# Kernel tuning notes

Measured on AMD Instinct MI355X. Metric: run time of the kernel, lower is better.

## Reference

```python
import jax, jax.numpy as jnp
import numpy as np
import math

D_MODEL = 384
D_HEAD = 64
N_HEADS = D_MODEL // D_HEAD  # 6
COND = 768
KSIZE = 7
EPS = 1e-6


def setup_inputs() -> dict:
    key = jax.random.key(0)
    ks = jax.random.split(key, 8)
    n, h, w = 4, 128, 128
    x = jax.random.normal(ks[0], (n, h, w, D_MODEL), jnp.float32)
    pos = jax.random.uniform(ks[1], (n, h, w, 2), jnp.float32)
    cond = jax.random.normal(ks[2], (n, COND), jnp.float32)
    # AdaRMSNorm linear (zero-init in original; small random so it exercises the math)
    w_cond = jax.random.normal(ks[3], (COND, D_MODEL), jnp.float32) * 0.02
    w_qkv = jax.random.normal(ks[4], (D_MODEL, 3 * D_MODEL), jnp.float32) * (D_MODEL ** -0.5)
    scale = jnp.full((N_HEADS,), 10.0, jnp.float32)
    # AxialRoPE freqs: exp(linspace(log(pi), log(10pi), n_heads*dim//4+1)[:-1]).view(dim//4, nh).T
    dim = D_HEAD // 2
    freqs = jnp.exp(jnp.linspace(math.log(math.pi), math.log(10.0 * math.pi),
                                 N_HEADS * (dim // 4) + 1)[:-1])
    freqs = freqs.reshape(dim // 4, N_HEADS).T  # [n_heads, d_head//8]
    w_out = jax.random.normal(ks[5], (D_MODEL, D_MODEL), jnp.float32) * 0.02
    return {"x": x, "pos": pos, "cond": cond, "w_cond": w_cond, "w_qkv": w_qkv,
            "scale": scale, "freqs": freqs, "w_out": w_out}


def rms_norm(x, scale):
    return x * jax.lax.rsqrt(jnp.mean(x * x, axis=-1, keepdims=True) + EPS) * scale


def apply_rotary(x, theta):
    # rotate the first 2*d channels of the head dim, leave the rest untouched
    d = theta.shape[-1]
    x1, x2, x3 = x[..., :d], x[..., d:2 * d], x[..., 2 * d:]
    c, s = jnp.cos(theta), jnp.sin(theta)
    return jnp.concatenate([x1 * c - x2 * s, x2 * c + x1 * s, x3], axis=-1)


def nb_idx(L):
    # NATTEN clamped neighborhood: window start = clip(i - k//2, 0, L-k)
    start = jnp.clip(jnp.arange(L) - KSIZE // 2, 0, L - KSIZE)
    return start[None, :] + jnp.arange(KSIZE)[:, None]  # [KSIZE, L]


def reference(x, pos, cond, w_cond, w_qkv, scale, freqs, w_out):
    n, H, W, _ = x.shape
    skip = x
    # AdaRMSNorm
    x = rms_norm(x, (cond @ w_cond)[:, None, None, :] + 1.0)
    # QKV projection, 'n h w (t nh e) -> t n nh h w e'
    qkv = (x @ w_qkv).reshape(n, H, W, 3, N_HEADS, D_HEAD)
    qkv = jnp.transpose(qkv, (3, 0, 4, 1, 2, 5))
    q, k, v = qkv[0], qkv[1], qkv[2]  # [n, nh, H, W, e]
    # cosine-sim scaling with learned per-head scale
    sq = jnp.sqrt(scale)[:, None, None, None]
    q = q * (sq * jax.lax.rsqrt(jnp.sum(q * q, axis=-1, keepdims=True) + EPS))
    k = k * (sq * jax.lax.rsqrt(jnp.sum(k * k, axis=-1, keepdims=True) + EPS))
    # axial RoPE: theta [n,H,W,nh,d_head//4] per axis -> cat -> movedim(-2,-4)
    th = pos[..., None, 0:1] * freqs
    tw = pos[..., None, 1:2] * freqs
    theta = jnp.moveaxis(jnp.concatenate([th, tw], axis=-1), -2, -4)  # [n,nh,H,W,dd]
    q = apply_rotary(q, theta)
    k = apply_rotary(k, theta)
    # neighborhood attention (na2d_qk / softmax / na2d_av), dilation 1
    ih_all = nb_idx(H)  # [k, H]
    iw_all = nb_idx(W)  # [k, W]
    hh = jnp.repeat(jnp.arange(KSIZE), KSIZE)
    ww = jnp.tile(jnp.arange(KSIZE), KSIZE)
    idx_h = ih_all[hh]  # [k*k, H]
    idx_w = iw_all[ww]  # [k*k, W]

    def qk_step(_, hw):
        ih, iw = hw
        ks_ = k[:, :, ih, :, :][:, :, :, iw, :]  # keys at this window offset
        return None, jnp.einsum('nchwe,nchwe->nchw', q, ks_)

    _, qk = jax.lax.scan(qk_step, None, (idx_h, idx_w))  # [k*k, n, nh, H, W]
    a = jax.nn.softmax(qk, axis=0)  # softmax over the k*k window

    def av_step(acc, inp):
        (ih, iw), at = inp
        vs = v[:, :, ih, :, :][:, :, :, iw, :]
        return acc + at[..., None] * vs, None

    out, _ = jax.lax.scan(av_step, jnp.zeros_like(v), ((idx_h, idx_w), a))
    # 'n nh h w e -> n h w (nh e)'
    out = jnp.transpose(out, (0, 2, 3, 1, 4)).reshape(n, H, W, N_HEADS * D_HEAD)
    return out @ w_out + skip
```

## Files before the change

### kernel.cpp

```cpp
#include <hip/hip_runtime.h>
#include <hip/hip_bf16.h>

#define DM 384
#define NH 6
#define DH 64
#define CD 768
#define NBATCH 4
#define IMH 128
#define IMW 128
#define HEADPIX (IMH*IMW)
#define NPIX (NBATCH*IMH*IMW)
#define PLANE ((size_t)NPIX*DM)
#define KS 7
#define EPSF 1e-6f

typedef __attribute__((ext_vector_type(8))) short bf16x8v;
typedef __attribute__((ext_vector_type(4))) short bf16x4v;
typedef __attribute__((ext_vector_type(4))) float f32x4v;
typedef __attribute__((ext_vector_type(4))) unsigned short u16x4;

#define GLOAD_LDS16(g, l) __builtin_amdgcn_global_load_lds( \
    (const __attribute__((address_space(1))) void*)(g), \
    (__attribute__((address_space(3))) void*)(l), 16, 0, 0)

#define TR64(dst, p, imm) asm volatile("ds_read_b64_tr_b16 %0, %1 offset:" #imm \
    : "=v"(dst) : "v"((const __attribute__((address_space(3))) char*)(p)))

__device__ __forceinline__ unsigned short f2bf(float f){
    __hip_bfloat16 h = __float2bfloat16(f);
    return *reinterpret_cast<unsigned short*>(&h);
}
__device__ __forceinline__ bf16x8v cat8(bf16x4v lo, bf16x4v hi){
    bf16x8v r;
    r[0]=lo[0]; r[1]=lo[1]; r[2]=lo[2]; r[3]=lo[3];
    r[4]=hi[0]; r[5]=hi[1]; r[6]=hi[2]; r[7]=hi[3];
    return r;
}

__device__ __forceinline__ bf16x8v frag8(const __hip_bfloat16* base, int row, int kelem){
    int byteoff = row*128 + ((kelem*2) ^ ((row & 7) << 4));
    return *(const bf16x8v*)((const char*)base + byteoff);
}
__device__ __forceinline__ bf16x8v frag512(const char* base, int row, int kelem){
    int byteoff = row*512 + ((kelem*2) ^ ((row & 7) << 4));
    return *(const bf16x8v*)(base + byteoff);
}

__global__ __launch_bounds__(256) void k_cond(const float* __restrict__ cond,
                                              const float* __restrict__ wc,
                                              float* __restrict__ sc){
    __shared__ float red[4][64];
    const int b = blockIdx.x;
    const int n = b / 6, j0 = (b - n*6) * 64;
    const int lane = threadIdx.x & 63, wave = threadIdx.x >> 6;
    const float* cr = cond + n*CD + wave*192;
    const float* wp = wc + (size_t)(wave*192)*DM + j0 + lane;
    float acc = 0.f;
    #pragma unroll 4
    for (int i = 0; i < 192; ++i) acc += cr[i] * wp[(size_t)i*DM];
    red[wave][lane] = acc;
    __syncthreads();
    if (threadIdx.x < 64) {
        float s = red[0][lane] + red[1][lane] + red[2][lane] + red[3][lane];
        sc[n*DM + j0 + lane] = s + 1.0f;
    }
}

__global__ __launch_bounds__(256) void k_xscale(const float* __restrict__ x,
                                                const float* __restrict__ sc,
                                                __hip_bfloat16* __restrict__ xb){
    int row  = blockIdx.x*4 + (threadIdx.x>>6);
    int lane = threadIdx.x & 63;
    int n    = row >> 14;
    const float* xr  = x + (size_t)row*DM;
    const float* scp = sc + n*DM;
    float v[6];
    float s = 0.f;
    #pragma unroll
    for (int i=0;i<6;++i){ v[i] = xr[i*64+lane]; s += v[i]*v[i]; }
    #pragma unroll
    for (int o=32;o;o>>=1) s += __shfl_xor(s,o);
    float r = rsqrtf(s*(1.0f/DM) + EPSF);
    #pragma unroll
    for (int i=0;i<6;++i)
        xb[(size_t)row*DM + i*64+lane] = __float2bfloat16(v[i]*r*scp[i*64+lane]);
}

__global__ void k_cvtwq(const float* __restrict__ wq, __hip_bfloat16* __restrict__ wqb){
    int id = blockIdx.x*256 + threadIdx.x;
    if (id >= 3*DM*DM) return;
    int nn = id / DM, kk = id - nn*DM;
    wqb[id] = __float2bfloat16(wq[(size_t)kk*(3*DM) + nn]);
}
__global__ void k_cvtwo(const float* __restrict__ wo, __hip_bfloat16* __restrict__ wob){
    int id = blockIdx.x*256 + threadIdx.x;
    if (id >= DM*DM) return;
    int nn = id / DM, kk = id - nn*DM;
    wob[id] = __float2bfloat16(wo[(size_t)kk*DM + nn]);
}

__global__ __launch_bounds__(256) void k_qkv_mfma(
    const __hip_bfloat16* __restrict__ xb, const __hip_bfloat16* __restrict__ wqb,
    const float* __restrict__ pos, const float* __restrict__ freqs,
    const float* __restrict__ scale, __hip_bfloat16* __restrict__ qkv)
{
    __shared__ char As[2*16384];
    __shared__ char Bs[2*16384];
    const int t    = threadIdx.x;
    const int lane = t & 63;
    const int wave = t >> 6;
    const int swzb = (blockIdx.x & 7)*576 + (blockIdx.x >> 3);
    const int jb = swzb % 9;
    const int mb = swzb / 9;
    const int j0 = jb*128, m0 = mb*128;
    const int n  = m0 >> 14;
    const int wr = (wave >> 1) * 64;
    const int wc = (wave & 1) * 64;
    const int fr = lane & 15;
    const int fg = lane >> 4;

    f32x4v acc[4][4] = {};

#define STAGE_QKV(buf, k0) \
    { _Pragma("unroll") \
      for (int i = 0; i < 4; ++i) { \
        int off = (i*256 + t) * 8; \
        int row = off >> 6; \
        int col = (off & 63) ^ ((row & 7) << 3); \
        GLOAD_LDS16(xb  + (size_t)(m0 + row)*DM + (k0) + col, \
                    As + (buf)*16384 + (i*256 + (wave<<6))*16); \
        GLOAD_LDS16(wqb + (size_t)(j0 + row)*DM + (k0) + col, \
                    Bs + (buf)*16384 + (i*256 + (wave<<6))*16); \
      } }

    STAGE_QKV(0, 0)
    #pragma unroll
    for (int kt = 0; kt < 6; ++kt) {
        const int cur = kt & 1;
        if (kt < 5) {
            STAGE_QKV(cur ^ 1, (kt+1)*64)
            asm volatile("s_waitcnt vmcnt(8)" ::: "memory");
        } else {
            asm volatile("s_waitcnt vmcnt(0)" ::: "memory");
        }
        asm volatile("s_barrier" ::: "memory");
        const __hip_bfloat16* Ab = (const __hip_bfloat16*)(As + cur*16384);
        const __hip_bfloat16* Bb = (const __hip_bfloat16*)(Bs + cur*16384);
        #pragma unroll
        for (int kk = 0; kk < 64; kk += 32) {
            bf16x8v af[4], bfr[4];
            #pragma unroll
            for (int i = 0; i < 4; ++i) af[i]  = frag8(Ab, wr + i*16 + fr, kk + fg*8);
            #pragma unroll
            for (int i = 0; i < 4; ++i) bfr[i] = frag8(Bb, wc + i*16 + fr, kk + fg*8);
            #pragma unroll
            for (int i = 0; i < 4; ++i)
            #pragma unroll
            for (int j = 0; j < 4; ++j)
                acc[i][j] = __builtin_amdgcn_mfma_f32_16x16x32_bf16(bfr[i], af[j], acc[i][j], 0, 0, 0);
        }
        asm volatile("s_barrier" ::: "memory");
    }
#undef STAGE_QKV

    const int t_ = jb / 3;
    const int pj = jb - t_*3;
    const int c  = pj*2 + (wc >> 6);
    const size_t hbase = (size_t)t_*PLANE + (((size_t)(n*NH + c)*HEADPIX) << 6);

    if (t_ < 2) {
        const float sq = sqrtf(scale[c]);
        const float4 f4 = *(const float4*)(freqs + c*8 + ((fg & 1) << 2));
        float fqv[4] = {f4.x, f4.y, f4.z, f4.w};
        #pragma unroll
        for (int ni = 0; ni < 4; ++ni) {
            int m = m0 + wr + ni*16 + fr;
            float ss = 0.f;
            #pragma unroll
            for (int i = 0; i < 4; ++i)
                #pragma unroll
                for (int r = 0; r < 4; ++r) ss += acc[i][ni][r]*acc[i][ni][r];
            ss += __shfl_xor(ss, 16);
            ss += __shfl_xor(ss, 32);
            float rn = sq * rsqrtf(ss + EPSF);
            float2 pp = *(const float2*)(pos + (size_t)m*2);
            float pc = (fg < 2) ? pp.x : pp.y;
            u16x4 o0, o1, o2, o3;
            #pragma unroll
            for (int r = 0; r < 4; ++r) {
                float th = pc * fqv[r];
                float ct = __cosf(th), st = __sinf(th);
                float a0 = acc[0][ni][r]*rn, a1 = acc[1][ni][r]*rn;
                o0[r] = f2bf(a0*ct - a1*st);
                o1[r] = f2bf(a1*ct + a0*st);
                o2[r] = f2bf(acc[2][ni][r]*rn);
                o3[r] = f2bf(acc[3][ni][r]*rn);
            }
            size_t base = hbase + ((size_t)(m & (HEADPIX-1)) << 6) + (fg << 2);
            *(u16x4*)(qkv + base     ) = o0;
            *(u16x4*)(qkv + base + 16) = o1;
            *(u16x4*)(qkv + base + 32) = o2;
            *(u16x4*)(qkv + base + 48) = o3;
        }
    } else {
        #pragma unroll
        for (int ni = 0; ni < 4; ++ni) {
            int m = m0 + wr + ni*16 + fr;
            size_t base = hbase + ((size_t)(m & (HEADPIX-1)) << 6) + (fg << 2);
            #pragma unroll
            for (int i = 0; i < 4; ++i) {
                u16x4 pk;
                #pragma unroll
                for (int r = 0; r < 4; ++r) pk[r] = f2bf(acc[i][ni][r]);
                *(u16x4*)(qkv + base + i*16) = pk;
            }
        }
    }
}

__global__ __launch_bounds__(256) void k_attn2(
    const __hip_bfloat16* __restrict__ q, const __hip_bfloat16* __restrict__ kbuf,
    const __hip_bfloat16* __restrict__ vbuf, __hip_bfloat16* __restrict__ attn)
{
    __shared__ char smem[61440];
    char* KP = smem;
    char* VT = smem + 32768;

    const int t    = threadIdx.x;
    const int lane = t & 63;
    const int wave = t >> 6;
    const int fr   = lane & 15;
    const int fg   = lane >> 4;

    const int tile = blockIdx.x;
    const int n6c  = blockIdx.y;
    const int h0 = (tile >> 4) << 3;
    const int w0 = (tile & 15) << 3;
    const int nn = n6c / NH;
    const int cc = n6c - nn*NH;

    const size_t pixbase = (size_t)n6c << 14;
    const __hip_bfloat16* qp = q    + (pixbase << 6);
    const __hip_bfloat16* kp = kbuf + (pixbase << 6);
    const __hip_bfloat16* vp = vbuf + (pixbase << 6);

    const int u0h = min(max(h0-3,0), IMH-7);
    const int u0w = min(max(w0-3,0), IMW-7);

    #pragma unroll
    for (int it = 0; it < 7; ++it) {
        int chunk = it*256 + t;
        int key  = chunk >> 3;
        int part = chunk & 7;
        int kh = min(u0h + (key >> 4), IMH-1);
        int kw = min(u0w + (key & 15), IMW-1);
        GLOAD_LDS16(kp + (((size_t)kh*IMW + kw) << 6) + ((part ^ (key & 7)) << 3),
                    KP + (it*256 + (wave<<6))*16);
    }
    #pragma unroll
    for (int it = 0; it < 7; ++it) {
        int chunk = it*256 + t;
        int keyq = chunk >> 5;
        int rem  = chunk & 31;
        int key  = (keyq << 2) + ((rem >> 1) & 3);
        int d0   = ((rem >> 3) << 4) + ((chunk & 1) << 3);
        int kh = min(u0h + (key >> 4), IMH-1);
        int kw = min(u0w + (key & 15), IMW-1);
        GLOAD_LDS16(vp + (((size_t)kh*IMW + kw) << 6) + d0,
                    VT + (it*256 + (wave<<6))*16);
    }
    const int q_l = (wave<<4) + fr;
    const int qh = h0 + (q_l >> 3), qw = w0 + (q_l & 7);
    const __hip_bfloat16* qrow = qp + (((size_t)qh*IMW + qw) << 6);
    bf16x8v aq0 = *(const bf16x8v*)(qrow + fg*8);
    bf16x8v aq1 = *(const bf16x8v*)(qrow + 32 + fg*8);

    int loh[4], low_[4];
    #pragma unroll
    for (int r = 0; r < 4; ++r) {
        int qr  = (wave<<4) + fg*4 + r;
        int qhr = h0 + (qr >> 3), qwr = w0 + (qr & 7);
        loh[r]  = min(max(qhr-3,0), IMH-7) - u0h;
        low_[r] = min(max(qwr-3,0), IMW-7) - u0w;
    }

    __syncthreads();

    f32x4v acc_s[14];
    #pragma unroll
    for (int nf = 0; nf < 14; ++nf) {
        bf16x8v b0 = frag8((const __hip_bfloat16*)KP, nf*16 + fr, fg*8);
        bf16x8v b1 = frag8((const __hip_bfloat16*)KP, nf*16 + fr, 32 + fg*8);
        f32x4v s = {0.f,0.f,0.f,0.f};
        s = __builtin_amdgcn_mfma_f32_16x16x32_bf16(aq0, b0, s, 0, 0, 0);
        s = __builtin_amdgcn_mfma_f32_16x16x32_bf16(aq1, b1, s, 0, 0, 0);
        acc_s[nf] = s;
    }

    float rs[4] = {0.f,0.f,0.f,0.f};
    #pragma unroll
    for (int nf = 0; nf < 14; ++nf) {
        int key = nf*16 + fr;
        int uh = key >> 4;
        int uw = key & 15;
        #pragma unroll
        for (int r = 0; r < 4; ++r) {
            bool ok = ((unsigned)(uh - loh[r]) <= 6u) && ((unsigned)(uw - low_[r]) <= 6u);
            float pv = ok ? __expf(acc_s[nf][r]) : 0.f;
            acc_s[nf][r] = pv;
            rs[r] += pv;
        }
    }
    #pragma unroll
    for (int o = 1; o < 16; o <<= 1) {
        #pragma unroll
        for (int r = 0; r < 4; ++r) rs[r] += __shfl_xor(rs[r], o);
    }
    float rinv[4];
    #pragma unroll
    for (int r = 0; r < 4; ++r) rinv[r] = 1.0f / rs[r];

    __syncthreads();

    #pragma unroll
    for (int nf = 0; nf < 14; ++nf) {
        int key = nf*16 + fr;
        #pragma unroll
        for (int r = 0; r < 4; ++r) {
            int qr = (wave<<4) + fg*4 + r;
            *(__hip_bfloat16*)(KP + qr*512 + ((key*2) ^ ((qr & 7) << 4))) = __float2bfloat16(acc_s[nf][r]);
        }
    }
    __syncthreads();

    f32x4v acc_o[4] = {};
    const char* vlane = VT + ((lane >> 4) << 10) + ((lane & 15) << 3);
    #pragma unroll
    for (int kst = 0; kst < 7; ++kst) {
        bf16x8v a = frag512(KP, (wave<<4) + fr, kst*32 + fg*8);
        const char* vk = vlane + kst*4096;
        bf16x4v t0a, t0b, t1a, t1b, t2a, t2b, t3a, t3b;
        TR64(t0a, vk,   0); TR64(t0b, vk, 512);
        TR64(t1a, vk, 128); TR64(t1b, vk, 640);
        TR64(t2a, vk, 256); TR64(t2b, vk, 768);
        TR64(t3a, vk, 384); TR64(t3b, vk, 896);
        asm volatile("s_waitcnt lgkmcnt(0)" ::: "memory");
        __builtin_amdgcn_sched_barrier(0);
        acc_o[0] = __builtin_amdgcn_mfma_f32_16x16x32_bf16(a, cat8(t0a,t0b), acc_o[0], 0, 0, 0);
        acc_o[1] = __builtin_amdgcn_mfma_f32_16x16x32_bf16(a, cat8(t1a,t1b), acc_o[1], 0, 0, 0);
        acc_o[2] = __builtin_amdgcn_mfma_f32_16x16x32_bf16(a, cat8(t2a,t2b), acc_o[2], 0, 0, 0);
        acc_o[3] = __builtin_amdgcn_mfma_f32_16x16x32_bf16(a, cat8(t3a,t3b), acc_o[3], 0, 0, 0);
    }

    #pragma unroll
    for (int nf = 0; nf < 4; ++nf) {
        int d = cc*64 + nf*16 + fr;
        #pragma unroll
        for (int r = 0; r < 4; ++r) {
            int qr  = (wave<<4) + fg*4 + r;
            int qhr = h0 + (qr >> 3), qwr = w0 + (qr & 7);
            size_t pix = ((size_t)nn << 14) + (size_t)qhr*IMW + qwr;
            attn[pix*DM + d] = __float2bfloat16(acc_o[nf][r] * rinv[r]);
        }
    }
}

__global__ __launch_bounds__(256) void k_out_mfma(
    const __hip_bfloat16* __restrict__ attn, const __hip_bfloat16* __restrict__ wob,
    const float* __restrict__ xin, float* __restrict__ out)
{
    __shared__ char As[2*16384];
    __shared__ char Bs[2*16384];
    const int t    = threadIdx.x;
    const int lane = t & 63;
    const int wave = t >> 6;
    const int swzb = (blockIdx.x & 7)*192 + (blockIdx.x >> 3);
    const int jb = swzb % 3;
    const int mb = swzb / 3;
    const int j0 = jb*128, m0 = mb*128;
    const int wr = (wave >> 1) * 64;
    const int wc = (wave & 1) * 64;
    const int fr = lane & 15;
    const int fg = lane >> 4;

    f32x4v acc[4][4] = {};

#define STAGE_OUT(buf, k0) \
    { _Pragma("unroll") \
      for (int i = 0; i < 4; ++i) { \
        int off = (i*256 + t) * 8; \
        int row = off >> 6; \
        int col = (off & 63) ^ ((row & 7) << 3); \
        GLOAD_LDS16(attn + (size_t)(m0 + row)*DM + (k0) + col, \
                    As + (buf)*16384 + (i*256 + (wave<<6))*16); \
        GLOAD_LDS16(wob  + (size_t)(j0 + row)*DM + (k0) + col, \
                    Bs + (buf)*16384 + (i*256 + (wave<<6))*16); \
      } }

    STAGE_OUT(0, 0)
    #pragma unroll
    for (int kt = 0; kt < 6; ++kt) {
        const int cur = kt & 1;
        if (kt < 5) {
            STAGE_OUT(cur ^ 1, (kt+1)*64)
            asm volatile("s_waitcnt vmcnt(8)" ::: "memory");
        } else {
            asm volatile("s_waitcnt vmcnt(0)" ::: "memory");
        }
        asm volatile("s_barrier" ::: "memory");
        const __hip_bfloat16* Ab = (const __hip_bfloat16*)(As + cur*16384);
        const __hip_bfloat16* Bb = (const __hip_bfloat16*)(Bs + cur*16384);
        #pragma unroll
        for (int kk = 0; kk < 64; kk += 32) {
            bf16x8v af[4], bfr[4];
            #pragma unroll
            for (int i = 0; i < 4; ++i) af[i]  = frag8(Ab, wr + i*16 + fr, kk + fg*8);
            #pragma unroll
            for (int i = 0; i < 4; ++i) bfr[i] = frag8(Bb, wc + i*16 + fr, kk + fg*8);
            #pragma unroll
            for (int i = 0; i < 4; ++i)
            #pragma unroll
            for (int j = 0; j < 4; ++j)
                acc[i][j] = __builtin_amdgcn_mfma_f32_16x16x32_bf16(bfr[i], af[j], acc[i][j], 0, 0, 0);
        }
        asm volatile("s_barrier" ::: "memory");
    }
#undef STAGE_OUT

    #pragma unroll
    for (int i = 0; i < 4; ++i) {
        int jg = j0 + wc + i*16 + (fg<<2);
        #pragma unroll
        for (int ni = 0; ni < 4; ++ni) {
            int m = m0 + wr + ni*16 + fr;
            size_t idx = (size_t)m*DM + jg;
            float4 xv = *(const float4*)(xin + idx);
            float4 ov;
            ov.x = acc[i][ni][0] + xv.x;
            ov.y = acc[i][ni][1] + xv.y;
            ov.z = acc[i][ni][2] + xv.z;
            ov.w = acc[i][ni][3] + xv.w;
            *(float4*)(out + idx) = ov;
        }
    }
}

extern "C" void kernel_launch(void* const* d_in, const int* in_sizes, int n_in,
                              void* d_out, int out_size, void* d_ws, size_t ws_size,
                              hipStream_t stream) {
    const float* x      = (const float*)d_in[0];
    const float* pos    = (const float*)d_in[1];
    const float* cond   = (const float*)d_in[2];
    const float* w_cond = (const float*)d_in[3];
    const float* w_qkv  = (const float*)d_in[4];
    const float* scale  = (const float*)d_in[5];
    const float* freqs  = (const float*)d_in[6];
    const float* w_out  = (const float*)d_in[7];
    float* out = (float*)d_out;

    char* ws = (char*)d_ws;
    __hip_bfloat16* xb   = (__hip_bfloat16*)ws;
    __hip_bfloat16* attn = (__hip_bfloat16*)ws;
    __hip_bfloat16* qkv  = (__hip_bfloat16*)(ws + 50331648);
    float* s_cond = (float*)(ws + 201326592);
    __hip_bfloat16* wqb = (__hip_bfloat16*)(ws + 201332736);
    __hip_bfloat16* qb = qkv;
    __hip_bfloat16* kb = qkv + PLANE;
    __hip_bfloat16* vb = qkv + 2*PLANE;
    __hip_bfloat16* wob = qkv;

    k_cvtwq<<<1728, 256, 0, stream>>>(w_qkv, wqb);
    k_cond<<<24, 256, 0, stream>>>(cond, w_cond, s_cond);
    k_xscale<<<NPIX/4, 256, 0, stream>>>(x, s_cond, xb);
    k_qkv_mfma<<<4608, 256, 0, stream>>>(xb, wqb, pos, freqs, scale, qkv);
    k_attn2<<<dim3(256, 24), 256, 0, stream>>>(qb, kb, vb, attn);
    k_cvtwo<<<576, 256, 0, stream>>>(w_out, wob);
    k_out_mfma<<<1536, 256, 0, stream>>>(attn, wob, x, out);
}
```

Before: 279.3 us.

## Single-buffer weight tiles in QKV and output GEMMs to cut LDS footprint

```diff
diff --git a/kernel.cpp b/kernel.cpp
--- a/kernel.cpp
+++ b/kernel.cpp
@@ -104,8 +104,8 @@
     const float* __restrict__ pos, const float* __restrict__ freqs,
     const float* __restrict__ scale, __hip_bfloat16* __restrict__ qkv)
 {
-    __shared__ char As[2*16384];
-    __shared__ char Bs[2*16384];
+    __shared__ __align__(16) char As[2*16384];
+    __shared__ __align__(16) char Bs[16384];
     const int t    = threadIdx.x;
     const int lane = t & 63;
     const int wave = t >> 6;
@@ -121,31 +121,36 @@
 
     f32x4v acc[4][4] = {};
 
-#define STAGE_QKV(buf, k0) \
+#define STAGE_A(buf, k0) \
     { _Pragma("unroll") \
       for (int i = 0; i < 4; ++i) { \
         int off = (i*256 + t) * 8; \
         int row = off >> 6; \
         int col = (off & 63) ^ ((row & 7) << 3); \
-        GLOAD_LDS16(xb  + (size_t)(m0 + row)*DM + (k0) + col, \
+        GLOAD_LDS16(xb + (size_t)(m0 + row)*DM + (k0) + col, \
                     As + (buf)*16384 + (i*256 + (wave<<6))*16); \
+      } }
+#define STAGE_B(k0) \
+    { _Pragma("unroll") \
+      for (int i = 0; i < 4; ++i) { \
+        int off = (i*256 + t) * 8; \
+        int row = off >> 6; \
+        int col = (off & 63) ^ ((row & 7) << 3); \
         GLOAD_LDS16(wqb + (size_t)(j0 + row)*DM + (k0) + col, \
-                    Bs + (buf)*16384 + (i*256 + (wave<<6))*16); \
+                    Bs + (i*256 + (wave<<6))*16); \
       } }
 
-    STAGE_QKV(0, 0)
+    STAGE_A(0, 0)
     #pragma unroll
     for (int kt = 0; kt < 6; ++kt) {
         const int cur = kt & 1;
-        if (kt < 5) {
-            STAGE_QKV(cur ^ 1, (kt+1)*64)
-            asm volatile("s_waitcnt vmcnt(8)" ::: "memory");
-        } else {
-            asm volatile("s_waitcnt vmcnt(0)" ::: "memory");
-        }
+        if (kt > 0) asm volatile("s_barrier" ::: "memory");
+        STAGE_B(kt*64)
+        asm volatile("s_waitcnt vmcnt(0)" ::: "memory");
         asm volatile("s_barrier" ::: "memory");
+        if (kt < 5) { STAGE_A(cur ^ 1, (kt+1)*64) }
         const __hip_bfloat16* Ab = (const __hip_bfloat16*)(As + cur*16384);
-        const __hip_bfloat16* Bb = (const __hip_bfloat16*)(Bs + cur*16384);
+        const __hip_bfloat16* Bb = (const __hip_bfloat16*)Bs;
         #pragma unroll
         for (int kk = 0; kk < 64; kk += 32) {
             bf16x8v af[4], bfr[4];
@@ -159,9 +164,9 @@
             for (int j = 0; j < 4; ++j)
                 acc[i][j] = __builtin_amdgcn_mfma_f32_16x16x32_bf16(bfr[i], af[j], acc[i][j], 0, 0, 0);
         }
-        asm volatile("s_barrier" ::: "memory");
-    }
-#undef STAGE_QKV
+    }
+#undef STAGE_A
+#undef STAGE_B
 
     const int t_ = jb / 3;
     const int pj = jb - t_*3;
@@ -369,8 +374,8 @@
     const __hip_bfloat16* __restrict__ attn, const __hip_bfloat16* __restrict__ wob,
     const float* __restrict__ xin, float* __restrict__ out)
 {
-    __shared__ char As[2*16384];
-    __shared__ char Bs[2*16384];
+    __shared__ __align__(16) char As[2*16384];
+    __shared__ __align__(16) char Bs[16384];
     const int t    = threadIdx.x;
     const int lane = t & 63;
     const int wave = t >> 6;
@@ -385,7 +390,7 @@
 
     f32x4v acc[4][4] = {};
 
-#define STAGE_OUT(buf, k0) \
+#define STAGE_A(buf, k0) \
     { _Pragma("unroll") \
       for (int i = 0; i < 4; ++i) { \
         int off = (i*256 + t) * 8; \
@@ -393,23 +398,28 @@
         int col = (off & 63) ^ ((row & 7) << 3); \
         GLOAD_LDS16(attn + (size_t)(m0 + row)*DM + (k0) + col, \
                     As + (buf)*16384 + (i*256 + (wave<<6))*16); \
-        GLOAD_LDS16(wob  + (size_t)(j0 + row)*DM + (k0) + col, \
-                    Bs + (buf)*16384 + (i*256 + (wave<<6))*16); \
       } }
-
-    STAGE_OUT(0, 0)
+#define STAGE_B(k0) \
+    { _Pragma("unroll") \
+      for (int i = 0; i < 4; ++i) { \
+        int off = (i*256 + t) * 8; \
+        int row = off >> 6; \
+        int col = (off & 63) ^ ((row & 7) << 3); \
+        GLOAD_LDS16(wob + (size_t)(j0 + row)*DM + (k0) + col, \
+                    Bs + (i*256 + (wave<<6))*16); \
+      } }
+
+    STAGE_A(0, 0)
     #pragma unroll
     for (int kt = 0; kt < 6; ++kt) {
         const int cur = kt & 1;
-        if (kt < 5) {
-            STAGE_OUT(cur ^ 1, (kt+1)*64)
-            asm volatile("s_waitcnt vmcnt(8)" ::: "memory");
-        } else {
-            asm volatile("s_waitcnt vmcnt(0)" ::: "memory");
-        }
+        if (kt > 0) asm volatile("s_barrier" ::: "memory");
+        STAGE_B(kt*64)
+        asm volatile("s_waitcnt vmcnt(0)" ::: "memory");
         asm volatile("s_barrier" ::: "memory");
+        if (kt < 5) { STAGE_A(cur ^ 1, (kt+1)*64) }
         const __hip_bfloat16* Ab = (const __hip_bfloat16*)(As + cur*16384);
-        const __hip_bfloat16* Bb = (const __hip_bfloat16*)(Bs + cur*16384);
+        const __hip_bfloat16* Bb = (const __hip_bfloat16*)Bs;
         #pragma unroll
         for (int kk = 0; kk < 64; kk += 32) {
             bf16x8v af[4], bfr[4];
@@ -423,9 +433,9 @@
             for (int j = 0; j < 4; ++j)
                 acc[i][j] = __builtin_amdgcn_mfma_f32_16x16x32_bf16(bfr[i], af[j], acc[i][j], 0, 0, 0);
         }
-        asm volatile("s_barrier" ::: "memory");
-    }
-#undef STAGE_OUT
+    }
+#undef STAGE_A
+#undef STAGE_B
 
     #pragma unroll
     for (int i = 0; i < 4; ++i) {
```

After: 303.3 us. 8.6% more time.
